# Kernel tuning notes

Hardware: AMD Instinct MI355X
Metric: run time of the kernel (lower is better)

## Reference

```python
import jax, jax.numpy as jnp
import numpy as np

TEMPERATURE = 0.5
NEG_FILL = -9e15


def setup_inputs() -> dict:
    key = jax.random.key(0)
    k1, k2 = jax.random.split(key)
    B, D = 4096, 256
    z_i = jax.random.normal(k1, (B, D), dtype=jnp.float32)
    z_j = jax.random.normal(k2, (B, D), dtype=jnp.float32)
    return {"z_i": z_i, "z_j": z_j}


def reference(z_i, z_j):
    B = z_i.shape[0]
    z = jnp.concatenate([z_i, z_j], axis=0)  # [2B, D]
    # L2 normalize rows (torch F.normalize uses eps=1e-12 clamp on norm)
    norm = jnp.maximum(jnp.linalg.norm(z, axis=1, keepdims=True), 1e-12)
    z_norm = z / norm
    sim = jnp.matmul(z_norm, z_norm.T) / TEMPERATURE  # [2B, 2B]
    n = 2 * B
    diag = jnp.eye(n, dtype=bool)
    sim = jnp.where(diag, NEG_FILL, sim)
    labels = jnp.concatenate([jnp.arange(B, 2 * B), jnp.arange(B)])
    logp = jax.nn.log_softmax(sim, axis=-1)
    loss = -jnp.mean(jnp.take_along_axis(logp, labels[:, None], axis=1))
    return loss
```

## Files before the change

kernel.cpp:

```cpp
#include <hip/hip_runtime.h>
#include <hip/hip_bf16.h>
#include <stdint.h>

#define N_TOT 8192
#define BHALF 4096
#define DIM   256
#define E2     7.38905609893065f
#define LOG2E2 2.8853900817779268f

typedef short s8v __attribute__((ext_vector_type(8)));
typedef float f4v __attribute__((ext_vector_type(4)));

static __device__ __forceinline__ unsigned short f2bf(float f) {
    union { float f; uint32_t u; } v; v.f = f;
    uint32_t r = (v.u + 0x7FFFu + ((v.u >> 16) & 1u)) >> 16;
    return (unsigned short)r;
}


__global__ __launch_bounds__(256) void nrm_kernel(const float* __restrict__ zi,
                                                  const float* __restrict__ zj,
                                                  s8v* __restrict__ zbF,
                                                  float* __restrict__ sumexp,
                                                  float* __restrict__ lab2) {
    const int wave = threadIdx.x >> 6;
    const int lane = threadIdx.x & 63;
    const int half = lane >> 5;
    const int sl   = lane & 31;
    const int p    = blockIdx.x * 4 + wave;
    const int row  = half ? (p + BHALF) : p;
    const float* src = (half ? zj : zi) + (size_t)p * DIM;

    float4 v0 = *(const float4*)(src + sl * 8);
    float4 v1 = *(const float4*)(src + sl * 8 + 4);
    float s = v0.x*v0.x + v0.y*v0.y + v0.z*v0.z + v0.w*v0.w
            + v1.x*v1.x + v1.y*v1.y + v1.z*v1.z + v1.w*v1.w;
    #pragma unroll
    for (int m = 1; m < 32; m <<= 1) s += __shfl_xor(s, m, 64);
    const float inv = 1.0f / fmaxf(sqrtf(s), 1e-12f);

    float n[8] = { v0.x*inv, v0.y*inv, v0.z*inv, v0.w*inv,
                   v1.x*inv, v1.y*inv, v1.z*inv, v1.w*inv };
    union { s8v v; unsigned short u[8]; } o;
    #pragma unroll
    for (int j = 0; j < 8; ++j) o.u[j] = f2bf(n[j]);
    zbF[(size_t)(((row >> 4) * 8 + (sl >> 2)) * 64) + (row & 15) + 16 * (sl & 3)] = o.v;

    float d = 0.f;
    #pragma unroll
    for (int j = 0; j < 8; ++j) d += n[j] * __shfl_xor(n[j], 32, 64);
    #pragma unroll
    for (int m = 1; m < 32; m <<= 1) d += __shfl_xor(d, m, 64);
    if (lane == 0) lab2[p] = 2.0f * d;

    if (threadIdx.x < 8) sumexp[blockIdx.x * 8 + threadIdx.x] = 0.f;
}

__global__ __launch_bounds__(256, 2) void sim_kernel(const s8v* __restrict__ zbF,
                                                     float* __restrict__ sumexp) {
    const int lane = threadIdx.x & 63;
    const int wave = threadIdx.x >> 6;
    const int rb   = blockIdx.x >> 4;
    const int cb   = blockIdx.x & 15;
    const int row0 = rb * 256 + wave * 64;
    const int ct0  = cb * 32;
    const int l15  = lane & 15;
    const int quad = lane >> 4;

    s8v a[4][8];
    #pragma unroll
    for (int rt = 0; rt < 4; ++rt) {
        const s8v* ap = zbF + (size_t)(((row0 >> 4) + rt) * 8) * 64 + lane;
        #pragma unroll
        for (int c = 0; c < 8; ++c) a[rt][c] = ap[c * 64];
    }
    #pragma unroll
    for (int rt = 0; rt < 4; ++rt)
        #pragma unroll
        for (int c = 0; c < 8; ++c)
            asm volatile("" : "+v"(a[rt][c]));

    float se[4][4];
    #pragma unroll
    for (int rt = 0; rt < 4; ++rt)
        #pragma unroll
        for (int r = 0; r < 4; ++r) se[rt][r] = 0.f;

    s8v b0[8], b1[8];
    {
        const s8v* bp = zbF + (size_t)(ct0 * 8) * 64 + lane;
        #pragma unroll
        for (int c = 0; c < 8; ++c) b0[c] = bp[c * 64];
    }

#define SIM_BODY(BCUR, BNXT, CT)                                                   \
    {                                                                              \
        const s8v* np = zbF + (size_t)((ct0 + (((CT) + 1) & 31)) * 8) * 64 + lane; \
        _Pragma("unroll")                                                          \
        for (int c = 0; c < 8; ++c) BNXT[c] = np[c * 64];                          \
        f4v acc[4];                                                                \
        _Pragma("unroll")                                                          \
        for (int rt = 0; rt < 4; ++rt) acc[rt] = (f4v){0.f, 0.f, 0.f, 0.f};       \
        _Pragma("unroll")                                                          \
        for (int c = 0; c < 8; ++c) {                                              \
            _Pragma("unroll")                                                      \
            for (int rt = 0; rt < 4; ++rt)                                         \
                acc[rt] = __builtin_amdgcn_mfma_f32_16x16x32_bf16(                 \
                    a[rt][c], BCUR[c], acc[rt], 0, 0, 0);                          \
        }                                                                          \
        _Pragma("unroll")                                                          \
        for (int rt = 0; rt < 4; ++rt)                                             \
            _Pragma("unroll")                                                      \
            for (int r = 0; r < 4; ++r)                                            \
                se[rt][r] += __builtin_amdgcn_exp2f(acc[rt][r] * LOG2E2);          \
    }

    #pragma unroll 1
    for (int ct = 0; ct < 32; ct += 2) {
        SIM_BODY(b0, b1, ct)
        SIM_BODY(b1, b0, ct + 1)
    }
#undef SIM_BODY

    #pragma unroll
    for (int rt = 0; rt < 4; ++rt) {
        #pragma unroll
        for (int r = 0; r < 4; ++r) {
            float s = se[rt][r];
            #pragma unroll
            for (int m = 1; m < 16; m <<= 1) s += __shfl_xor(s, m, 64);
            if (l15 == 0)
                atomicAdd(&sumexp[row0 + rt*16 + quad*4 + r], s);
        }
    }
}

__global__ __launch_bounds__(256) void fin_kernel(const float* __restrict__ sumexp,
                                                  const float* __restrict__ lab2,
                                                  float* __restrict__ out) {
    const int tid = threadIdx.x;
    float acc = 0.f;
    for (int i = tid; i < N_TOT; i += 256)
        acc += logf(sumexp[i] - E2);
    for (int p = tid; p < BHALF; p += 256)
        acc -= 2.0f * lab2[p];
    #pragma unroll
    for (int m = 1; m < 64; m <<= 1) acc += __shfl_xor(acc, m, 64);
    __shared__ float wsum[4];
    if ((tid & 63) == 0) wsum[tid >> 6] = acc;
    __syncthreads();
    if (tid == 0) out[0] = (wsum[0] + wsum[1] + wsum[2] + wsum[3]) / (float)N_TOT;
}

extern "C" void kernel_launch(void* const* d_in, const int* in_sizes, int n_in,
                              void* d_out, int out_size, void* d_ws, size_t ws_size,
                              hipStream_t stream) {
    const float* zi = (const float*)d_in[0];
    const float* zj = (const float*)d_in[1];
    s8v* zbF = (s8v*)d_ws;
    float* sumexp = (float*)((char*)d_ws + (size_t)N_TOT * DIM * 2);
    float* lab2   = sumexp + N_TOT;

    nrm_kernel<<<1024, 256, 0, stream>>>(zi, zj, zbF, sumexp, lab2);
    sim_kernel<<<512, 256, 0, stream>>>(zbF, sumexp);
    fin_kernel<<<1, 256, 0, stream>>>(sumexp, lab2, (float*)d_out);
}
```

Before: 111.5 us.

## Exploit similarity matrix symmetry by computing only upper-triangular tiles

Since the similarity matrix is symmetric, each block now computes a 128x128 tile only when its column index is at least its row index. Off-diagonal tiles add their exponentials to both the row sums and, through per-column atomics, the column sums. This roughly halves the MFMA and exp work. In exchange the grid becomes 4096 mostly small blocks, half of which exit immediately. It also adds many more atomic additions and drops the double-buffered B prefetch.

```diff
diff --git a/kernel.cpp b/kernel.cpp
--- a/kernel.cpp
+++ b/kernel.cpp
@@ -56,74 +56,65 @@
     if (threadIdx.x < 8) sumexp[blockIdx.x * 8 + threadIdx.x] = 0.f;
 }
 
-__global__ __launch_bounds__(256, 2) void sim_kernel(const s8v* __restrict__ zbF,
+__global__ __launch_bounds__(256, 3) void sim_kernel(const s8v* __restrict__ zbF,
                                                      float* __restrict__ sumexp) {
+    const int tr = blockIdx.x >> 6;
+    const int tc = blockIdx.x & 63;
+    if (tc < tr) return;
     const int lane = threadIdx.x & 63;
     const int wave = threadIdx.x >> 6;
-    const int rb   = blockIdx.x >> 4;
-    const int cb   = blockIdx.x & 15;
-    const int row0 = rb * 256 + wave * 64;
-    const int ct0  = cb * 32;
+    const int row0 = tr * 128 + wave * 32;
+    const int cf0  = tc * 8;
     const int l15  = lane & 15;
     const int quad = lane >> 4;
+    const bool offdiag = (tr != tc);
 
-    s8v a[4][8];
+    s8v a[2][8];
     #pragma unroll
-    for (int rt = 0; rt < 4; ++rt) {
+    for (int rt = 0; rt < 2; ++rt) {
         const s8v* ap = zbF + (size_t)(((row0 >> 4) + rt) * 8) * 64 + lane;
         #pragma unroll
         for (int c = 0; c < 8; ++c) a[rt][c] = ap[c * 64];
     }
-    #pragma unroll
-    for (int rt = 0; rt < 4; ++rt)
+
+    float se[2][4] = {{0.f,0.f,0.f,0.f},{0.f,0.f,0.f,0.f}};
+
+    #pragma unroll 1
+    for (int ct = 0; ct < 8; ++ct) {
+        const s8v* bp = zbF + (size_t)((cf0 + ct) * 8) * 64 + lane;
+        s8v b[8];
         #pragma unroll
-        for (int c = 0; c < 8; ++c)
-            asm volatile("" : "+v"(a[rt][c]));
+        for (int c = 0; c < 8; ++c) b[c] = bp[c * 64];
 
-    float se[4][4];
-    #pragma unroll
-    for (int rt = 0; rt < 4; ++rt)
+        f4v acc[2];
+        acc[0] = (f4v){0.f,0.f,0.f,0.f};
+        acc[1] = (f4v){0.f,0.f,0.f,0.f};
         #pragma unroll
-        for (int r = 0; r < 4; ++r) se[rt][r] = 0.f;
+        for (int c = 0; c < 8; ++c) {
+            acc[0] = __builtin_amdgcn_mfma_f32_16x16x32_bf16(a[0][c], b[c], acc[0], 0, 0, 0);
+            acc[1] = __builtin_amdgcn_mfma_f32_16x16x32_bf16(a[1][c], b[c], acc[1], 0, 0, 0);
+        }
 
-    s8v b0[8], b1[8];
-    {
-        const s8v* bp = zbF + (size_t)(ct0 * 8) * 64 + lane;
+        float cl = 0.f;
         #pragma unroll
-        for (int c = 0; c < 8; ++c) b0[c] = bp[c * 64];
+        for (int rt = 0; rt < 2; ++rt) {
+            #pragma unroll
+            for (int r = 0; r < 4; ++r) {
+                const float e = __builtin_amdgcn_exp2f(acc[rt][r] * LOG2E2);
+                se[rt][r] += e;
+                cl += e;
+            }
+        }
+        if (offdiag) {
+            cl += __shfl_xor(cl, 16, 64);
+            cl += __shfl_xor(cl, 32, 64);
+            if (quad == 0)
+                atomicAdd(&sumexp[(cf0 + ct) * 16 + l15], cl);
+        }
     }
 
-#define SIM_BODY(BCUR, BNXT, CT)                                                   \
-    {                                                                              \
-        const s8v* np = zbF + (size_t)((ct0 + (((CT) + 1) & 31)) * 8) * 64 + lane; \
-        _Pragma("unroll")                                                          \
-        for (int c = 0; c < 8; ++c) BNXT[c] = np[c * 64];                          \
-        f4v acc[4];                                                                \
-        _Pragma("unroll")                                                          \
-        for (int rt = 0; rt < 4; ++rt) acc[rt] = (f4v){0.f, 0.f, 0.f, 0.f};       \
-        _Pragma("unroll")                                                          \
-        for (int c = 0; c < 8; ++c) {                                              \
-            _Pragma("unroll")                                                      \
-            for (int rt = 0; rt < 4; ++rt)                                         \
-                acc[rt] = __builtin_amdgcn_mfma_f32_16x16x32_bf16(                 \
-                    a[rt][c], BCUR[c], acc[rt], 0, 0, 0);                          \
-        }                                                                          \
-        _Pragma("unroll")                                                          \
-        for (int rt = 0; rt < 4; ++rt)                                             \
-            _Pragma("unroll")                                                      \
-            for (int r = 0; r < 4; ++r)                                            \
-                se[rt][r] += __builtin_amdgcn_exp2f(acc[rt][r] * LOG2E2);          \
-    }
-
-    #pragma unroll 1
-    for (int ct = 0; ct < 32; ct += 2) {
-        SIM_BODY(b0, b1, ct)
-        SIM_BODY(b1, b0, ct + 1)
-    }
-#undef SIM_BODY
-
     #pragma unroll
-    for (int rt = 0; rt < 4; ++rt) {
+    for (int rt = 0; rt < 2; ++rt) {
         #pragma unroll
         for (int r = 0; r < 4; ++r) {
             float s = se[rt][r];
@@ -162,6 +153,6 @@
     float* lab2   = sumexp + N_TOT;
 
     nrm_kernel<<<1024, 256, 0, stream>>>(zi, zj, zbF, sumexp, lab2);
-    sim_kernel<<<512, 256, 0, stream>>>(zbF, sumexp);
+    sim_kernel<<<4096, 256, 0, stream>>>(zbF, sumexp);
     fin_kernel<<<1, 256, 0, stream>>>(sumexp, lab2, (float*)d_out);
 }
```

Measured after the change: 125.5 us. 1.13x slower.
